# Optimization experiments

Hardware: AMD Instinct MI355X
Metric: run time of the kernel (lower is better)

The kernel has to match this reference:

```python
import jax, jax.numpy as jnp
import numpy as np

EPS = 1e-5  # torch nn.LayerNorm default


def layer_norm(x, g, b):
    mu = jnp.mean(x, axis=-1, keepdims=True)
    var = jnp.mean(jnp.square(x - mu), axis=-1, keepdims=True)
    return (x - mu) * jax.lax.rsqrt(var + EPS) * g + b


def run_dir(g_ih_seq, w_hh, g_hh, b_hh, g_ho, b_ho, reverse):
    """Run one LayerNormLSTMCell direction over precomputed LN(x @ W_ih^T).
    g_ih_seq: [S, B, 4H]. Returns final hidden [B, H]."""
    S, B, G = g_ih_seq.shape
    H = G // 4

    def step(carry, gih_t):
        h, c = carry
        gates = gih_t + layer_norm(h @ w_hh.T, g_hh, b_hh)  # [B, 4H]
        i, f, o = jnp.split(jax.nn.sigmoid(gates[:, : 3 * H]), 3, axis=1)
        g = jnp.tanh(gates[:, 3 * H :])
        c = f * c + i * g
        h = o * jnp.tanh(layer_norm(c, g_ho, b_ho))
        return (h, c), None

    z = jnp.zeros((B, H), g_ih_seq.dtype)
    (hT, _), _ = jax.lax.scan(step, (z, z), g_ih_seq, reverse=reverse)
    return hT


def lnlstm(x, w_ih0, w_hh0, ln_ih0_g, ln_ih0_b, ln_hh0_g, ln_hh0_b, ln_ho0_g,
           ln_ho0_b, w_ih1, w_hh1, ln_ih1_g, ln_ih1_b, ln_hh1_g, ln_hh1_b,
           ln_ho1_g, ln_ho1_b):
    # x: [B, S, E] -> permute(1,0,2)
    x_seq = jnp.transpose(x, (1, 0, 2))  # [S, B, E]
    S, B, _ = x_seq.shape

    # ---- layer 0 (time-varying input) ----
    g0f = layer_norm(jnp.einsum('sbe,ge->sbg', x_seq, w_ih0[0]), ln_ih0_g[0], ln_ih0_b[0])
    hf = run_dir(g0f, w_hh0[0], ln_hh0_g[0], ln_hh0_b[0], ln_ho0_g[0], ln_ho0_b[0], False)
    g0b = layer_norm(jnp.einsum('sbe,ge->sbg', x_seq, w_ih0[1]), ln_ih0_g[1], ln_ih0_b[1])
    hb = run_dir(g0b, w_hh0[1], ln_hh0_g[1], ln_hh0_b[1], ln_ho0_g[1], ln_ho0_b[1], True)

    # Due to the `[[None]*N]*seq_len` aliasing bug in the original torch code,
    # the next layer's input is the SAME vector at every timestep:
    xc = jnp.concatenate([hf, hb], axis=1)  # [B, 2H]

    # ---- layer 1 (constant input; LN(x@W_ih^T) computed once, broadcast over time) ----
    g1f = layer_norm(xc @ w_ih1[0].T, ln_ih1_g[0], ln_ih1_b[0])
    hf1 = run_dir(jnp.broadcast_to(g1f, (S,) + g1f.shape), w_hh1[0],
                  ln_hh1_g[0], ln_hh1_b[0], ln_ho1_g[0], ln_ho1_b[0], False)
    g1b = layer_norm(xc @ w_ih1[1].T, ln_ih1_g[1], ln_ih1_b[1])
    hb1 = run_dir(jnp.broadcast_to(g1b, (S,) + g1b.shape), w_hh1[1],
                  ln_hh1_g[1], ln_hh1_b[1], ln_ho1_g[1], ln_ho1_b[1], True)

    # y = max over time of identical vectors == the vector itself
    return jnp.concatenate([hf1, hb1], axis=1)  # [B, 2H]


def setup_inputs() -> dict:
    key = jax.random.key(0)
    ks = jax.random.split(key, 20)
    B, S, E, H = 64, 48, 512, 512
    f = jnp.float32
    n = jax.random.normal
    u = jax.random.uniform
    return {
        'x': n(ks[0], (B, S, E), f),
        'text_length': jax.random.randint(ks[1], (B,), 1, S),
        'w_ih0': n(ks[2], (2, 4 * H, E), f) * 0.05,
        'w_hh0': n(ks[3], (2, 4 * H, H), f) * 0.05,
        'ln_ih0_g': u(ks[4], (2, 4 * H), f, 0.5, 1.5),
        'ln_ih0_b': n(ks[5], (2, 4 * H), f) * 0.02,
        'ln_hh0_g': u(ks[6], (2, 4 * H), f, 0.5, 1.5),
        'ln_hh0_b': n(ks[7], (2, 4 * H), f) * 0.02,
        'ln_ho0_g': u(ks[8], (2, H), f, 0.5, 1.5),
        'ln_ho0_b': n(ks[9], (2, H), f) * 0.02,
        'w_ih1': n(ks[10], (2, 4 * H, 2 * H), f) * 0.05,
        'w_hh1': n(ks[11], (2, 4 * H, H), f) * 0.05,
        'ln_ih1_g': u(ks[12], (2, 4 * H), f, 0.5, 1.5),
        'ln_ih1_b': n(ks[13], (2, 4 * H), f) * 0.02,
        'ln_hh1_g': u(ks[14], (2, 4 * H), f, 0.5, 1.5),
        'ln_hh1_b': n(ks[15], (2, 4 * H), f) * 0.02,
        'ln_ho1_g': u(ks[16], (2, H), f, 0.5, 1.5),
        'ln_ho1_b': n(ks[17], (2, H), f) * 0.02,
    }


def reference(x, text_length, w_ih0, w_hh0, ln_ih0_g, ln_ih0_b, ln_hh0_g,
              ln_hh0_b, ln_ho0_g, ln_ho0_b, w_ih1, w_hh1, ln_ih1_g, ln_ih1_b,
              ln_hh1_g, ln_hh1_b, ln_ho1_g, ln_ho1_b):
    # text_length is accepted but unused by the original forward
    return lnlstm(x, w_ih0, w_hh0, ln_ih0_g, ln_ih0_b, ln_hh0_g, ln_hh0_b,
                  ln_ho0_g, ln_ho0_b, w_ih1, w_hh1, ln_ih1_g, ln_ih1_b,
                  ln_hh1_g, ln_hh1_b, ln_ho1_g, ln_ho1_b)
```

## Files before the change

kernel.cpp:

```cpp
#include <hip/hip_runtime.h>
#include <math.h>

#define HH 512
#define BB 64
#define SS 48
#define EE 512
#define G4 2048
#define EPSF 1e-5f
#define AGENT __HIP_MEMORY_SCOPE_AGENT
typedef unsigned long long ull;

__device__ __forceinline__ float aload(const float* p) {
  return __hip_atomic_load(p, __ATOMIC_RELAXED, AGENT);
}
__device__ __forceinline__ void astore(float* p, float v) {
  __hip_atomic_store(p, v, __ATOMIC_RELAXED, AGENT);
}
__device__ __forceinline__ float2 aloadf2(const float2* p) {
  ull u = __hip_atomic_load((const ull*)p, __ATOMIC_RELAXED, AGENT);
  union { ull u; float2 f; } x; x.u = u; return x.f;
}
__device__ __forceinline__ void astoref2(float2* p, float2 v) {
  union { ull u; float2 f; } x; x.f = v;
  __hip_atomic_store((ull*)p, x.u, __ATOMIC_RELAXED, AGENT);
}

__device__ __forceinline__ float fsig(float x) {
  x = fminf(fmaxf(x, -30.f), 30.f);
  return 1.f / (1.f + __expf(-x));
}
__device__ __forceinline__ float ftanh(float x) {
  float e = __expf(fminf(fmaxf(2.f*x, -60.f), 60.f));
  return (e - 1.f) / (e + 1.f);
}

__device__ __forceinline__ void wdetect(const int* f, int target) {
  int spins = 0;
  for (;;) {
    int v = __hip_atomic_load(f + (threadIdx.x & 31)*32, __ATOMIC_RELAXED, AGENT);
    #pragma unroll
    for (int off = 16; off > 0; off >>= 1) v = min(v, __shfl_xor(v, off, 32));
    if (v >= target) break;
    __builtin_amdgcn_s_sleep(1);
    if (++spins > (1 << 22)) break;
  }
}

__device__ __forceinline__ void gsync(int* c, int target) {
  __builtin_amdgcn_s_waitcnt(0);
  __syncthreads();
  if (threadIdx.x == 0) {
    __hip_atomic_fetch_add(c, 1, __ATOMIC_RELEASE, AGENT);
    int spins = 0;
    while (__hip_atomic_load(c, __ATOMIC_RELAXED, AGENT) < target) {
      __builtin_amdgcn_s_sleep(2);
      if (++spins > (1 << 21)) break;
    }
    (void)__hip_atomic_load(c, __ATOMIC_ACQUIRE, AGENT);
  }
  __syncthreads();
}

__global__ __launch_bounds__(256)
void gemm_ih0(const float* __restrict__ x, const float* __restrict__ w_ih0,
              float* __restrict__ G0) {
  __shared__ float As[16][65];
  __shared__ float Bs[16][65];
  const int m0 = blockIdx.y * 64;
  const int d  = m0 / (BB * SS);
  const float* Wm = w_ih0 + (size_t)d * G4 * EE;
  const int bn = blockIdx.x * 64;
  const int tid = threadIdx.x;
  const int lrow = tid >> 2;
  const int lkk  = (tid & 3) << 2;
  const int tx = tid & 15;
  const int ty = tid >> 4;
  int m  = m0 + lrow;
  int r  = m - d * (BB * SS);
  int b  = r / SS;
  int tl = r - b * SS;
  int s  = d ? (SS - 1 - tl) : tl;
  const float* arow = x + ((size_t)b * SS + s) * EE;

  float acc[4][4] = {};
  for (int k0 = 0; k0 < EE; k0 += 16) {
    float4 av = *(const float4*)(arow + k0 + lkk);
    float4 bv = *(const float4*)(Wm + (size_t)(bn + lrow) * EE + k0 + lkk);
    As[lkk+0][lrow] = av.x; As[lkk+1][lrow] = av.y; As[lkk+2][lrow] = av.z; As[lkk+3][lrow] = av.w;
    Bs[lkk+0][lrow] = bv.x; Bs[lkk+1][lrow] = bv.y; Bs[lkk+2][lrow] = bv.z; Bs[lkk+3][lrow] = bv.w;
    __syncthreads();
    #pragma unroll
    for (int k = 0; k < 16; ++k) {
      float a[4], bbv[4];
      #pragma unroll
      for (int i = 0; i < 4; ++i) a[i] = As[k][ty*4+i];
      #pragma unroll
      for (int j = 0; j < 4; ++j) bbv[j] = Bs[k][tx*4+j];
      #pragma unroll
      for (int i = 0; i < 4; ++i)
        #pragma unroll
        for (int j = 0; j < 4; ++j) acc[i][j] += a[i]*bbv[j];
    }
    __syncthreads();
  }
  for (int i = 0; i < 4; ++i)
    for (int j = 0; j < 4; ++j)
      G0[(size_t)(m0 + ty*4 + i) * G4 + bn + tx*4 + j] = acc[i][j];
}

__global__ __launch_bounds__(256)
void ln_rows(float* __restrict__ X, const float* __restrict__ gamma,
             const float* __restrict__ beta, int rows_per_d) {
  __shared__ float red[8];
  const int row = blockIdx.x;
  const int d = row / rows_per_d;
  float* xr = X + (size_t)row * G4;
  const float* gg = gamma + (size_t)d * G4;
  const float* bb = beta  + (size_t)d * G4;
  float s = 0.f, q = 0.f;
  float v[8];
  #pragma unroll
  for (int it = 0; it < 8; ++it) {
    float xv = xr[threadIdx.x + it*256];
    v[it] = xv; s += xv; q += xv*xv;
  }
  #pragma unroll
  for (int off = 32; off > 0; off >>= 1) { s += __shfl_down(s, off); q += __shfl_down(q, off); }
  int lane = threadIdx.x & 63, wid = threadIdx.x >> 6;
  if (lane == 0) { red[wid] = s; red[4+wid] = q; }
  __syncthreads();
  float ts = red[0]+red[1]+red[2]+red[3];
  float tq = red[4]+red[5]+red[6]+red[7];
  float mu = ts * (1.f/G4);
  float rstd = rsqrtf(tq*(1.f/G4) - mu*mu + EPSF);
  #pragma unroll
  for (int it = 0; it < 8; ++it) {
    int jc = threadIdx.x + it*256;
    xr[jc] = (v[it]-mu)*rstd*gg[jc] + bb[jc];
  }
}

__global__ __launch_bounds__(1024, 4)
void persist8(const float* __restrict__ whh, const float* __restrict__ Gbuf,
              long g_row_stride, long g_t_stride,
              const float* __restrict__ lnhg, const float* __restrict__ lnhb,
              const float* __restrict__ lnog, const float* __restrict__ lnob,
              float2* cobuf, float2* Rpart, float2* Cpart,
              int* flagsA, int* flagsB,
              float* fout, int nsteps,
              int mode1, const float* __restrict__ w_ih1,
              const float* __restrict__ xcb, float* g1pre,
              const float* __restrict__ ln_g1, const float* __restrict__ ln_b1,
              int* cnt_pre) {
  __shared__ float hlds[16][1024];
  __shared__ float part[16][8][64];
  __shared__ float redR[16][64];
  __shared__ float sred[32];

  const int bb = blockIdx.x;
  const int tid = threadIdx.x;
  const int l = tid & 63;

  if (mode1) {
    const int dp = bb & 1, nbp = bb >> 1;
    const int pb = tid >> 4, ns = tid & 15;
    const int col = nbp*16 + ns;
    const float* xrow = xcb + (size_t)pb * 1024;
    const float* wv_ = w_ih1 + ((size_t)dp*G4 + col) * 1024;
    float a = 0.f;
    for (int k = 0; k < 1024; k += 4) {
      float4 xv = *(const float4*)(xrow + k);
      float4 wv4 = *(const float4*)(wv_ + k);
      a += xv.x*wv4.x + xv.y*wv4.y + xv.z*wv4.z + xv.w*wv4.w;
    }
    astore(g1pre + ((size_t)dp*BB + pb) * G4 + col, a);
    gsync(cnt_pre + 0, 256);
    if (bb < 128) {
      const int ld = bb >> 6;
      float* xr = g1pre + (size_t)bb * G4;
      const float* gg = ln_g1 + (size_t)ld * G4;
      const float* be = ln_b1 + (size_t)ld * G4;
      float v0 = aload(xr + tid), v1 = aload(xr + tid + 1024);
      float s = v0 + v1, q = v0*v0 + v1*v1;
      #pragma unroll
      for (int off = 32; off > 0; off >>= 1) { s += __shfl_down(s, off); q += __shfl_down(q, off); }
      const int wv2 = tid >> 6;
      if (l == 0) { sred[wv2] = s; sred[16+wv2] = q; }
      __syncthreads();
      float ts = 0.f, tq = 0.f;
      #pragma unroll
      for (int i = 0; i < 16; ++i) { ts += sred[i]; tq += sred[16+i]; }
      float mu = ts * (1.f/G4);
      float rstd = rsqrtf(tq*(1.f/G4) - mu*mu + EPSF);
      astore(xr + tid,        (v0-mu)*rstd*gg[tid]      + be[tid]);
      astore(xr + tid + 1024, (v1-mu)*rstd*gg[tid+1024] + be[tid+1024]);
    }
    gsync(cnt_pre + 16, 256);
  }

  const int g  = bb & 7;
  const int d  = g >> 2;
  const int bq = g & 3;
  const int jb = bb >> 3;
  const int rowbase = d*BB + bq*16;
  const int ke = tid >> 6;
  const int ncol = jb*16 + ((l>>4) << 9) + (l & 15);
  int* fA = flagsA + g*1024;
  int* fB = flagsB + g*1024;

  float wreg[32];
  {
    const float* wp = whh + ((size_t)d*G4 + ncol)*HH + (size_t)ke*32;
    #pragma unroll
    for (int i = 0; i < 32; ++i) wreg[i] = wp[i];
  }

  const int bl = tid >> 4, jl = tid & 15;
  const int rowc = rowbase + bl;
  const int jc = jb*16 + jl;
  const int scol = tid & 511, srh = tid >> 9;
  const float ogv = lnog[(size_t)d*HH + scol];
  const float obv = lnob[(size_t)d*HH + scol];
  const int row16 = tid >> 5, j32 = tid & 31;
  const int inv_g = (g_t_stride == 0);
  const int strow = rowbase + ((l >> 3) << 1) + srh;
  const int stslot = (l & 7) * 4;

  float hg0=0,hg1=0,hg2=0,hg3=0, hb0=0,hb1=0,hb2=0,hb3=0;
  float cg0=0,cg1=0,cg2=0,cg3=0;
  if (tid < 256) {
    const float* lnhg_d = lnhg + (size_t)d*G4;
    const float* lnhb_d = lnhb + (size_t)d*G4;
    hg0 = lnhg_d[jc];        hb0 = lnhb_d[jc];
    hg1 = lnhg_d[HH+jc];     hb1 = lnhb_d[HH+jc];
    hg2 = lnhg_d[2*HH+jc];   hb2 = lnhb_d[2*HH+jc];
    hg3 = lnhg_d[3*HH+jc];   hb3 = lnhb_d[3*HH+jc];
    if (inv_g) {
      const float* gr = Gbuf + (size_t)rowc * g_row_stride;
      cg0 = gr[jc]; cg1 = gr[HH+jc]; cg2 = gr[2*HH+jc]; cg3 = gr[3*HH+jc];
    }
  }
  float creg = 0.f;

  for (int t = 0; t < nsteps; ++t) {
    wdetect(fB, t);
    {
      float2 co[8];
      #pragma unroll
      for (int i = 0; i < 8; ++i)
        co[i] = aloadf2(cobuf + (size_t)(rowbase + i*2 + srh)*512 + scol);
      float s = 0.f, q = 0.f;
      #pragma unroll
      for (int m = 0; m < 4; ++m) {
        float2 p = aloadf2(Cpart + (size_t)strow*32 + stslot + m);
        s += p.x; q += p.y;
      }
      #pragma unroll
      for (int off = 4; off > 0; off >>= 1) { s += __shfl_xor(s, off, 8); q += __shfl_xor(q, off, 8); }
      #pragma unroll
      for (int i = 0; i < 8; ++i) {
        float si = __shfl(s, i*8, 64);
        float qi = __shfl(q, i*8, 64);
        float mu = si * (1.f/HH);
        float rs = rsqrtf(qi*(1.f/HH) - mu*mu + EPSF);
        hlds[i*2 + srh][scol] = co[i].y * ftanh((co[i].x - mu)*rs*ogv + obv);
      }
    }
    __syncthreads();

    #pragma unroll
    for (int half = 0; half < 2; ++half) {
      #pragma unroll
      for (int b = 0; b < 8; ++b) {
        const float* hp = &hlds[half*8 + b][ke*32];
        float acc = 0.f;
        #pragma unroll
        for (int i4 = 0; i4 < 8; ++i4) {
          float4 h4 = *(const float4*)(hp + 4*i4);
          acc += h4.x*wreg[4*i4+0] + h4.y*wreg[4*i4+1]
               + h4.z*wreg[4*i4+2] + h4.w*wreg[4*i4+3];
        }
        part[ke][b][l] = acc;
      }
      __syncthreads();
      if (tid < 512) {
        int b = tid >> 6, n2 = tid & 63;
        float r = 0.f;
        #pragma unroll
        for (int k16 = 0; k16 < 16; ++k16) r += part[k16][b][n2];
        redR[half*8 + b][n2] = r;
      }
      __syncthreads();
    }
    if (tid < 512) {
      float v1 = redR[row16][j32], v2 = redR[row16][j32+32];
      float s = v1 + v2, q = v1*v1 + v2*v2;
      #pragma unroll
      for (int off = 16; off > 0; off >>= 1) { s += __shfl_down(s, off, 32); q += __shfl_down(q, off, 32); }
      if (j32 == 0)
        astoref2(Rpart + (size_t)(rowbase+row16)*32 + jb, make_float2(s, q));
    }
    float pg0 = cg0, pg1 = cg1, pg2 = cg2, pg3 = cg3;
    if (tid < 256 && !inv_g) {
      const float* gr = Gbuf + (size_t)rowc * g_row_stride + (size_t)t * g_t_stride;
      pg0 = gr[jc]; pg1 = gr[HH+jc]; pg2 = gr[2*HH+jc]; pg3 = gr[3*HH+jc];
    }
    __syncthreads();
    if (tid == 0) __hip_atomic_store(fA + jb*32, t + 1, __ATOMIC_RELAXED, AGENT);

    if (tid < 256) {
      wdetect(fA, t + 1);
      float2 pa = aloadf2(Rpart + (size_t)rowc*32 + jl);
      float2 pb = aloadf2(Rpart + (size_t)rowc*32 + jl + 16);
      float s2 = pa.x + pb.x, q2 = pa.y + pb.y;
      #pragma unroll
      for (int off = 8; off > 0; off >>= 1) { s2 += __shfl_xor(s2, off, 16); q2 += __shfl_xor(q2, off, 16); }
      float mu = s2 * (1.f/G4);
      float rstd = rsqrtf(q2*(1.f/G4) - mu*mu + EPSF);
      float gi = pg0 + (redR[bl][jl]    - mu)*rstd*hg0 + hb0;
      float gf = pg1 + (redR[bl][16+jl] - mu)*rstd*hg1 + hb1;
      float go = pg2 + (redR[bl][32+jl] - mu)*rstd*hg2 + hb2;
      float gt = pg3 + (redR[bl][48+jl] - mu)*rstd*hg3 + hb3;
      float iv = fsig(gi), fv = fsig(gf), ov = fsig(go), gv = ftanh(gt);
      creg = fv*creg + iv*gv;
      float cs = creg, cq = creg*creg;
      #pragma unroll
      for (int off = 8; off > 0; off >>= 1) { cs += __shfl_xor(cs, off, 16); cq += __shfl_xor(cq, off, 16); }
      if (jl == 0)
        astoref2(Cpart + (size_t)rowc*32 + jb, make_float2(cs, cq));
      astoref2(cobuf + (size_t)rowc*512 + jc, make_float2(creg, ov));
    }
    __syncthreads();
    if (tid == 0) __hip_atomic_store(fB + jb*32, t + 1, __ATOMIC_RELAXED, AGENT);
  }

  if (jb == 0) {
    wdetect(fB, nsteps);
    float2 co[8];
    #pragma unroll
    for (int i = 0; i < 8; ++i)
      co[i] = aloadf2(cobuf + (size_t)(rowbase + i*2 + srh)*512 + scol);
    float s = 0.f, q = 0.f;
    #pragma unroll
    for (int m = 0; m < 4; ++m) {
      float2 p = aloadf2(Cpart + (size_t)strow*32 + stslot + m);
      s += p.x; q += p.y;
    }
    #pragma unroll
    for (int off = 4; off > 0; off >>= 1) { s += __shfl_xor(s, off, 8); q += __shfl_xor(q, off, 8); }
    #pragma unroll
    for (int i = 0; i < 8; ++i) {
      float si = __shfl(s, i*8, 64);
      float qi = __shfl(q, i*8, 64);
      float mu = si * (1.f/HH);
      float rs = rsqrtf(qi*(1.f/HH) - mu*mu + EPSF);
      int row = i*2 + srh;
      float h = co[i].y * ftanh((co[i].x - mu)*rs*ogv + obv);
      fout[(size_t)(bq*16 + row) * 1024 + (size_t)d*512 + scol] = h;
    }
  }
}

extern "C" void kernel_launch(void* const* d_in, const int* in_sizes, int n_in,
                              void* d_out, int out_size, void* d_ws, size_t ws_size,
                              hipStream_t stream) {
  const float* x        = (const float*)d_in[0];
  const float* w_ih0    = (const float*)d_in[2];
  const float* w_hh0    = (const float*)d_in[3];
  const float* ln_ih0_g = (const float*)d_in[4];
  const float* ln_ih0_b = (const float*)d_in[5];
  const float* ln_hh0_g = (const float*)d_in[6];
  const float* ln_hh0_b = (const float*)d_in[7];
  const float* ln_ho0_g = (const float*)d_in[8];
  const float* ln_ho0_b = (const float*)d_in[9];
  const float* w_ih1    = (const float*)d_in[10];
  const float* w_hh1    = (const float*)d_in[11];
  const float* ln_ih1_g = (const float*)d_in[12];
  const float* ln_ih1_b = (const float*)d_in[13];
  const float* ln_hh1_g = (const float*)d_in[14];
  const float* ln_hh1_b = (const float*)d_in[15];
  const float* ln_ho1_g = (const float*)d_in[16];
  const float* ln_ho1_b = (const float*)d_in[17];
  float* out = (float*)d_out;

  float*  G0    = (float*)d_ws;
  float*  g1pre = G0 + (size_t)2*BB*SS*G4;
  float*  xcb   = g1pre + (size_t)2*BB*G4;
  float2* Rpart = (float2*)(xcb + (size_t)BB*1024);
  float2* Cpart = Rpart + (size_t)128*32;
  float2* cobuf = Cpart + (size_t)128*32;
  int*    ints  = (int*)(cobuf + (size_t)128*512);
  int*    fA0     = ints;
  int*    fB0     = ints + 8192;
  int*    fA1     = ints + 16384;
  int*    fB1     = ints + 24576;
  int*    cnt_pre = ints + 32768;

  hipMemsetAsync(Cpart, 0, ((size_t)128*32 + (size_t)128*512)*sizeof(float2)
                           + 32832*sizeof(int), stream);

  hipLaunchKernelGGL(gemm_ih0, dim3(G4/64, (2*BB*SS)/64), dim3(256), 0, stream,
      x, w_ih0, G0);
  hipLaunchKernelGGL(ln_rows, dim3(2*BB*SS), dim3(256), 0, stream,
      G0, ln_ih0_g, ln_ih0_b, BB*SS);

  hipLaunchKernelGGL(persist8, dim3(256), dim3(1024), 0, stream,
      w_hh0, G0, (long)SS*G4, (long)G4,
      ln_hh0_g, ln_hh0_b, ln_ho0_g, ln_ho0_b,
      cobuf, Rpart, Cpart, fA0, fB0, xcb, SS,
      0, (const float*)nullptr, (const float*)nullptr, (float*)nullptr,
      (const float*)nullptr, (const float*)nullptr, (int*)nullptr);

  hipMemsetAsync(Cpart, 0, ((size_t)128*32 + (size_t)128*512)*sizeof(float2), stream);

  hipLaunchKernelGGL(persist8, dim3(256), dim3(1024), 0, stream,
      w_hh1, g1pre, (long)G4, 0L,
      ln_hh1_g, ln_hh1_b, ln_ho1_g, ln_ho1_b,
      cobuf, Rpart, Cpart, fA1, fB1, out, SS,
      1, w_ih1, xcb, g1pre, ln_ih1_g, ln_ih1_b, cnt_pre);
}
```

Measured before the change: 1.896 ms.

## Split each block's work across both directions to overlap phase-A barrier latency

Each persistent block now handles 8 batch rows from each of the two LSTM directions instead of 16 rows from one direction. It keeps both directions' recurrent weight slices in registers. Each step runs the forward-direction matvec and publishes its partial stats with flag fA0, then does the backward-direction matvec while that flag propagates, so the grid-wide wait is hidden behind useful work. The cost is twice the weight registers per thread (risking spills or lower occupancy at 1024 threads), more __syncthreads per step, and a larger flag layout.

```diff
diff --git a/kernel.cpp b/kernel.cpp
--- a/kernel.cpp
+++ b/kernel.cpp
@@ -141,20 +141,21 @@
 }
 
 __global__ __launch_bounds__(1024, 4)
-void persist8(const float* __restrict__ whh, const float* __restrict__ Gbuf,
+void persist9(const float* __restrict__ whh, const float* __restrict__ Gbuf,
               long g_row_stride, long g_t_stride,
               const float* __restrict__ lnhg, const float* __restrict__ lnhb,
               const float* __restrict__ lnog, const float* __restrict__ lnob,
               float2* cobuf, float2* Rpart, float2* Cpart,
-              int* flagsA, int* flagsB,
-              float* fout, int nsteps,
+              int* flags, float* fout, int nsteps,
               int mode1, const float* __restrict__ w_ih1,
               const float* __restrict__ xcb, float* g1pre,
               const float* __restrict__ ln_g1, const float* __restrict__ ln_b1,
               int* cnt_pre) {
-  __shared__ float hlds[16][1024];
+  __shared__ float hlds0[8][1024];
+  __shared__ float hlds1[8][1024];
   __shared__ float part[16][8][64];
-  __shared__ float redR[16][64];
+  __shared__ float redR0[8][64];
+  __shared__ float redR1[8][64];
   __shared__ float sred[32];
 
   const int bb = blockIdx.x;
@@ -199,45 +200,48 @@
   }
 
   const int g  = bb & 7;
-  const int d  = g >> 2;
-  const int bq = g & 3;
   const int jb = bb >> 3;
-  const int rowbase = d*BB + bq*16;
+  const int brow0 = g*8;
+  const int brow1 = 64 + g*8;
   const int ke = tid >> 6;
   const int ncol = jb*16 + ((l>>4) << 9) + (l & 15);
-  int* fA = flagsA + g*1024;
-  int* fB = flagsB + g*1024;
-
-  float wreg[32];
+  int* fA0 = flags + g*3072;
+  int* fA1 = fA0 + 1024;
+  int* fB  = fA0 + 2048;
+
+  float wreg0[32], wreg1[32];
   {
-    const float* wp = whh + ((size_t)d*G4 + ncol)*HH + (size_t)ke*32;
-    #pragma unroll
-    for (int i = 0; i < 32; ++i) wreg[i] = wp[i];
-  }
-
-  const int bl = tid >> 4, jl = tid & 15;
-  const int rowc = rowbase + bl;
-  const int jc = jb*16 + jl;
+    const float* wp0 = whh + (size_t)ncol*HH + (size_t)ke*32;
+    const float* wp1 = whh + (size_t)(G4 + ncol)*HH + (size_t)ke*32;
+    #pragma unroll
+    for (int i = 0; i < 32; ++i) { wreg0[i] = wp0[i]; wreg1[i] = wp1[i]; }
+  }
+
   const int scol = tid & 511, srh = tid >> 9;
-  const float ogv = lnog[(size_t)d*HH + scol];
-  const float obv = lnob[(size_t)d*HH + scol];
-  const int row16 = tid >> 5, j32 = tid & 31;
+  const float ogv0 = lnog[scol],      obv0 = lnob[scol];
+  const float ogv1 = lnog[HH + scol], obv1 = lnob[HH + scol];
+  const int strow = l >> 3;
+  const int stslot = (l & 7) * 4;
   const int inv_g = (g_t_stride == 0);
-  const int strow = rowbase + ((l >> 3) << 1) + srh;
-  const int stslot = (l & 7) * 4;
-
+
+  int urowc = 0, ujc = 0, ubl = 0, ujl = 0;
   float hg0=0,hg1=0,hg2=0,hg3=0, hb0=0,hb1=0,hb2=0,hb3=0;
   float cg0=0,cg1=0,cg2=0,cg3=0;
   if (tid < 256) {
-    const float* lnhg_d = lnhg + (size_t)d*G4;
-    const float* lnhb_d = lnhb + (size_t)d*G4;
-    hg0 = lnhg_d[jc];        hb0 = lnhb_d[jc];
-    hg1 = lnhg_d[HH+jc];     hb1 = lnhb_d[HH+jc];
-    hg2 = lnhg_d[2*HH+jc];   hb2 = lnhb_d[2*HH+jc];
-    hg3 = lnhg_d[3*HH+jc];   hb3 = lnhb_d[3*HH+jc];
+    const int ud = tid >> 7;
+    const int u = tid & 127;
+    ubl = u >> 4; ujl = u & 15;
+    urowc = ud*64 + g*8 + ubl;
+    ujc = jb*16 + ujl;
+    const float* hgp = lnhg + (size_t)ud*G4;
+    const float* hbp = lnhb + (size_t)ud*G4;
+    hg0 = hgp[ujc];        hb0 = hbp[ujc];
+    hg1 = hgp[HH+ujc];     hb1 = hbp[HH+ujc];
+    hg2 = hgp[2*HH+ujc];   hb2 = hbp[2*HH+ujc];
+    hg3 = hgp[3*HH+ujc];   hb3 = hbp[3*HH+ujc];
     if (inv_g) {
-      const float* gr = Gbuf + (size_t)rowc * g_row_stride;
-      cg0 = gr[jc]; cg1 = gr[HH+jc]; cg2 = gr[2*HH+jc]; cg3 = gr[3*HH+jc];
+      const float* gr = Gbuf + (size_t)urowc * g_row_stride;
+      cg0 = gr[ujc]; cg1 = gr[HH+ujc]; cg2 = gr[2*HH+ujc]; cg3 = gr[3*HH+ujc];
     }
   }
   float creg = 0.f;
@@ -245,90 +249,142 @@
   for (int t = 0; t < nsteps; ++t) {
     wdetect(fB, t);
     {
-      float2 co[8];
-      #pragma unroll
-      for (int i = 0; i < 8; ++i)
-        co[i] = aloadf2(cobuf + (size_t)(rowbase + i*2 + srh)*512 + scol);
-      float s = 0.f, q = 0.f;
+      float2 co[4]; float s = 0.f, q = 0.f;
+      #pragma unroll
+      for (int i = 0; i < 4; ++i)
+        co[i] = aloadf2(cobuf + (size_t)(brow0 + i*2 + srh)*512 + scol);
       #pragma unroll
       for (int m = 0; m < 4; ++m) {
-        float2 p = aloadf2(Cpart + (size_t)strow*32 + stslot + m);
+        float2 p = aloadf2(Cpart + (size_t)(brow0 + strow)*32 + stslot + m);
         s += p.x; q += p.y;
       }
       #pragma unroll
       for (int off = 4; off > 0; off >>= 1) { s += __shfl_xor(s, off, 8); q += __shfl_xor(q, off, 8); }
       #pragma unroll
-      for (int i = 0; i < 8; ++i) {
-        float si = __shfl(s, i*8, 64);
-        float qi = __shfl(q, i*8, 64);
+      for (int i = 0; i < 4; ++i) {
+        int r = i*2 + srh;
+        float si = __shfl(s, r*8, 64), qi = __shfl(q, r*8, 64);
         float mu = si * (1.f/HH);
         float rs = rsqrtf(qi*(1.f/HH) - mu*mu + EPSF);
-        hlds[i*2 + srh][scol] = co[i].y * ftanh((co[i].x - mu)*rs*ogv + obv);
-      }
-    }
-    __syncthreads();
-
-    #pragma unroll
-    for (int half = 0; half < 2; ++half) {
-      #pragma unroll
-      for (int b = 0; b < 8; ++b) {
-        const float* hp = &hlds[half*8 + b][ke*32];
-        float acc = 0.f;
-        #pragma unroll
-        for (int i4 = 0; i4 < 8; ++i4) {
-          float4 h4 = *(const float4*)(hp + 4*i4);
-          acc += h4.x*wreg[4*i4+0] + h4.y*wreg[4*i4+1]
-               + h4.z*wreg[4*i4+2] + h4.w*wreg[4*i4+3];
-        }
-        part[ke][b][l] = acc;
-      }
-      __syncthreads();
-      if (tid < 512) {
-        int b = tid >> 6, n2 = tid & 63;
-        float r = 0.f;
-        #pragma unroll
-        for (int k16 = 0; k16 < 16; ++k16) r += part[k16][b][n2];
-        redR[half*8 + b][n2] = r;
-      }
-      __syncthreads();
-    }
+        hlds0[r][scol] = co[i].y * ftanh((co[i].x - mu)*rs*ogv0 + obv0);
+      }
+    }
+    __syncthreads();
+    #pragma unroll
+    for (int b = 0; b < 8; ++b) {
+      const float* hp = &hlds0[b][ke*32];
+      float acc = 0.f;
+      #pragma unroll
+      for (int i4 = 0; i4 < 8; ++i4) {
+        float4 h4 = *(const float4*)(hp + 4*i4);
+        acc += h4.x*wreg0[4*i4+0] + h4.y*wreg0[4*i4+1]
+             + h4.z*wreg0[4*i4+2] + h4.w*wreg0[4*i4+3];
+      }
+      part[ke][b][l] = acc;
+    }
+    __syncthreads();
     if (tid < 512) {
-      float v1 = redR[row16][j32], v2 = redR[row16][j32+32];
+      int b = tid >> 6, n2 = tid & 63;
+      float r = 0.f;
+      #pragma unroll
+      for (int k16 = 0; k16 < 16; ++k16) r += part[k16][b][n2];
+      redR0[b][n2] = r;
+    }
+    __syncthreads();
+    if (tid < 256) {
+      int row8 = tid >> 5, j32 = tid & 31;
+      float v1 = redR0[row8][j32], v2 = redR0[row8][j32+32];
       float s = v1 + v2, q = v1*v1 + v2*v2;
       #pragma unroll
       for (int off = 16; off > 0; off >>= 1) { s += __shfl_down(s, off, 32); q += __shfl_down(q, off, 32); }
       if (j32 == 0)
-        astoref2(Rpart + (size_t)(rowbase+row16)*32 + jb, make_float2(s, q));
+        astoref2(Rpart + (size_t)(brow0 + row8)*32 + jb, make_float2(s, q));
     }
     float pg0 = cg0, pg1 = cg1, pg2 = cg2, pg3 = cg3;
     if (tid < 256 && !inv_g) {
-      const float* gr = Gbuf + (size_t)rowc * g_row_stride + (size_t)t * g_t_stride;
-      pg0 = gr[jc]; pg1 = gr[HH+jc]; pg2 = gr[2*HH+jc]; pg3 = gr[3*HH+jc];
-    }
-    __syncthreads();
-    if (tid == 0) __hip_atomic_store(fA + jb*32, t + 1, __ATOMIC_RELAXED, AGENT);
-
+      const float* gr = Gbuf + (size_t)urowc * g_row_stride + (size_t)t * g_t_stride;
+      pg0 = gr[ujc]; pg1 = gr[HH+ujc]; pg2 = gr[2*HH+ujc]; pg3 = gr[3*HH+ujc];
+    }
+    __syncthreads();
+    if (tid == 0) __hip_atomic_store(fA0 + jb*32, t + 1, __ATOMIC_RELAXED, AGENT);
+
+    {
+      float2 co[4]; float s = 0.f, q = 0.f;
+      #pragma unroll
+      for (int i = 0; i < 4; ++i)
+        co[i] = aloadf2(cobuf + (size_t)(brow1 + i*2 + srh)*512 + scol);
+      #pragma unroll
+      for (int m = 0; m < 4; ++m) {
+        float2 p = aloadf2(Cpart + (size_t)(brow1 + strow)*32 + stslot + m);
+        s += p.x; q += p.y;
+      }
+      #pragma unroll
+      for (int off = 4; off > 0; off >>= 1) { s += __shfl_xor(s, off, 8); q += __shfl_xor(q, off, 8); }
+      #pragma unroll
+      for (int i = 0; i < 4; ++i) {
+        int r = i*2 + srh;
+        float si = __shfl(s, r*8, 64), qi = __shfl(q, r*8, 64);
+        float mu = si * (1.f/HH);
+        float rs = rsqrtf(qi*(1.f/HH) - mu*mu + EPSF);
+        hlds1[r][scol] = co[i].y * ftanh((co[i].x - mu)*rs*ogv1 + obv1);
+      }
+    }
+    __syncthreads();
+    #pragma unroll
+    for (int b = 0; b < 8; ++b) {
+      const float* hp = &hlds1[b][ke*32];
+      float acc = 0.f;
+      #pragma unroll
+      for (int i4 = 0; i4 < 8; ++i4) {
+        float4 h4 = *(const float4*)(hp + 4*i4);
+        acc += h4.x*wreg1[4*i4+0] + h4.y*wreg1[4*i4+1]
+             + h4.z*wreg1[4*i4+2] + h4.w*wreg1[4*i4+3];
+      }
+      part[ke][b][l] = acc;
+    }
+    __syncthreads();
+    if (tid < 512) {
+      int b = tid >> 6, n2 = tid & 63;
+      float r = 0.f;
+      #pragma unroll
+      for (int k16 = 0; k16 < 16; ++k16) r += part[k16][b][n2];
+      redR1[b][n2] = r;
+    }
+    __syncthreads();
     if (tid < 256) {
-      wdetect(fA, t + 1);
-      float2 pa = aloadf2(Rpart + (size_t)rowc*32 + jl);
-      float2 pb = aloadf2(Rpart + (size_t)rowc*32 + jl + 16);
-      float s2 = pa.x + pb.x, q2 = pa.y + pb.y;
+      int row8 = tid >> 5, j32 = tid & 31;
+      float v1 = redR1[row8][j32], v2 = redR1[row8][j32+32];
+      float s = v1 + v2, q = v1*v1 + v2*v2;
+      #pragma unroll
+      for (int off = 16; off > 0; off >>= 1) { s += __shfl_down(s, off, 32); q += __shfl_down(q, off, 32); }
+      if (j32 == 0)
+        astoref2(Rpart + (size_t)(brow1 + row8)*32 + jb, make_float2(s, q));
+    }
+    __syncthreads();
+    if (tid == 0) __hip_atomic_store(fA1 + jb*32, t + 1, __ATOMIC_RELAXED, AGENT);
+
+    if (tid < 256) {
+      const float (*redR)[64] = (tid < 128) ? redR0 : redR1;
+      wdetect((tid < 128) ? fA0 : fA1, t + 1);
+      float2 pa = aloadf2(Rpart + (size_t)urowc*32 + ujl);
+      float2 pb2 = aloadf2(Rpart + (size_t)urowc*32 + ujl + 16);
+      float s2 = pa.x + pb2.x, q2 = pa.y + pb2.y;
       #pragma unroll
       for (int off = 8; off > 0; off >>= 1) { s2 += __shfl_xor(s2, off, 16); q2 += __shfl_xor(q2, off, 16); }
       float mu = s2 * (1.f/G4);
       float rstd = rsqrtf(q2*(1.f/G4) - mu*mu + EPSF);
-      float gi = pg0 + (redR[bl][jl]    - mu)*rstd*hg0 + hb0;
-      float gf = pg1 + (redR[bl][16+jl] - mu)*rstd*hg1 + hb1;
-      float go = pg2 + (redR[bl][32+jl] - mu)*rstd*hg2 + hb2;
-      float gt = pg3 + (redR[bl][48+jl] - mu)*rstd*hg3 + hb3;
+      float gi = pg0 + (redR[ubl][ujl]    - mu)*rstd*hg0 + hb0;
+      float gf = pg1 + (redR[ubl][16+ujl] - mu)*rstd*hg1 + hb1;
+      float go = pg2 + (redR[ubl][32+ujl] - mu)*rstd*hg2 + hb2;
+      float gt = pg3 + (redR[ubl][48+ujl] - mu)*rstd*hg3 + hb3;
       float iv = fsig(gi), fv = fsig(gf), ov = fsig(go), gv = ftanh(gt);
       creg = fv*creg + iv*gv;
       float cs = creg, cq = creg*creg;
       #pragma unroll
       for (int off = 8; off > 0; off >>= 1) { cs += __shfl_xor(cs, off, 16); cq += __shfl_xor(cq, off, 16); }
-      if (jl == 0)
-        astoref2(Cpart + (size_t)rowc*32 + jb, make_float2(cs, cq));
-      astoref2(cobuf + (size_t)rowc*512 + jc, make_float2(creg, ov));
+      if (ujl == 0)
+        astoref2(Cpart + (size_t)urowc*32 + jb, make_float2(cs, cq));
+      astoref2(cobuf + (size_t)urowc*512 + ujc, make_float2(creg, ov));
     }
     __syncthreads();
     if (tid == 0) __hip_atomic_store(fB + jb*32, t + 1, __ATOMIC_RELAXED, AGENT);
@@ -336,27 +392,31 @@
 
   if (jb == 0) {
     wdetect(fB, nsteps);
-    float2 co[8];
-    #pragma unroll
-    for (int i = 0; i < 8; ++i)
-      co[i] = aloadf2(cobuf + (size_t)(rowbase + i*2 + srh)*512 + scol);
-    float s = 0.f, q = 0.f;
-    #pragma unroll
-    for (int m = 0; m < 4; ++m) {
-      float2 p = aloadf2(Cpart + (size_t)strow*32 + stslot + m);
-      s += p.x; q += p.y;
-    }
-    #pragma unroll
-    for (int off = 4; off > 0; off >>= 1) { s += __shfl_xor(s, off, 8); q += __shfl_xor(q, off, 8); }
-    #pragma unroll
-    for (int i = 0; i < 8; ++i) {
-      float si = __shfl(s, i*8, 64);
-      float qi = __shfl(q, i*8, 64);
-      float mu = si * (1.f/HH);
-      float rs = rsqrtf(qi*(1.f/HH) - mu*mu + EPSF);
-      int row = i*2 + srh;
-      float h = co[i].y * ftanh((co[i].x - mu)*rs*ogv + obv);
-      fout[(size_t)(bq*16 + row) * 1024 + (size_t)d*512 + scol] = h;
+    #pragma unroll
+    for (int dd = 0; dd < 2; ++dd) {
+      const int base = dd*64 + g*8;
+      const float og = dd ? ogv1 : ogv0;
+      const float ob = dd ? obv1 : obv0;
+      float2 co[4]; float s = 0.f, q = 0.f;
+      #pragma unroll
+      for (int i = 0; i < 4; ++i)
+        co[i] = aloadf2(cobuf + (size_t)(base + i*2 + srh)*512 + scol);
+      #pragma unroll
+      for (int m = 0; m < 4; ++m) {
+        float2 p = aloadf2(Cpart + (size_t)(base + strow)*32 + stslot + m);
+        s += p.x; q += p.y;
+      }
+      #pragma unroll
+      for (int off = 4; off > 0; off >>= 1) { s += __shfl_xor(s, off, 8); q += __shfl_xor(q, off, 8); }
+      #pragma unroll
+      for (int i = 0; i < 4; ++i) {
+        int r = i*2 + srh;
+        float si = __shfl(s, r*8, 64), qi = __shfl(q, r*8, 64);
+        float mu = si * (1.f/HH);
+        float rs = rsqrtf(qi*(1.f/HH) - mu*mu + EPSF);
+        float h = co[i].y * ftanh((co[i].x - mu)*rs*og + ob);
+        fout[(size_t)(g*8 + r)*1024 + (size_t)dd*512 + scol] = h;
+      }
     }
   }
 }
@@ -390,32 +450,30 @@
   float2* Cpart = Rpart + (size_t)128*32;
   float2* cobuf = Cpart + (size_t)128*32;
   int*    ints  = (int*)(cobuf + (size_t)128*512);
-  int*    fA0     = ints;
-  int*    fB0     = ints + 8192;
-  int*    fA1     = ints + 16384;
-  int*    fB1     = ints + 24576;
-  int*    cnt_pre = ints + 32768;
+  int*    flagsL0 = ints;
+  int*    flagsL1 = ints + 24576;
+  int*    cnt_pre = ints + 49152;
 
   hipMemsetAsync(Cpart, 0, ((size_t)128*32 + (size_t)128*512)*sizeof(float2)
-                           + 32832*sizeof(int), stream);
+                           + (49152 + 64)*sizeof(int), stream);
 
   hipLaunchKernelGGL(gemm_ih0, dim3(G4/64, (2*BB*SS)/64), dim3(256), 0, stream,
       x, w_ih0, G0);
   hipLaunchKernelGGL(ln_rows, dim3(2*BB*SS), dim3(256), 0, stream,
       G0, ln_ih0_g, ln_ih0_b, BB*SS);
 
-  hipLaunchKernelGGL(persist8, dim3(256), dim3(1024), 0, stream,
+  hipLaunchKernelGGL(persist9, dim3(256), dim3(1024), 0, stream,
       w_hh0, G0, (long)SS*G4, (long)G4,
       ln_hh0_g, ln_hh0_b, ln_ho0_g, ln_ho0_b,
-      cobuf, Rpart, Cpart, fA0, fB0, xcb, SS,
+      cobuf, Rpart, Cpart, flagsL0, xcb, SS,
       0, (const float*)nullptr, (const float*)nullptr, (float*)nullptr,
       (const float*)nullptr, (const float*)nullptr, (int*)nullptr);
 
   hipMemsetAsync(Cpart, 0, ((size_t)128*32 + (size_t)128*512)*sizeof(float2), stream);
 
-  hipLaunchKernelGGL(persist8, dim3(256), dim3(1024), 0, stream,
+  hipLaunchKernelGGL(persist9, dim3(256), dim3(1024), 0, stream,
       w_hh1, g1pre, (long)G4, 0L,
       ln_hh1_g, ln_hh1_b, ln_ho1_g, ln_ho1_b,
-      cobuf, Rpart, Cpart, fA1, fB1, out, SS,
+      cobuf, Rpart, Cpart, flagsL1, out, SS,
       1, w_ih1, xcb, g1pre, ln_ih1_g, ln_ih1_b, cnt_pre);
 }
```

New measurement: 2.714 ms. 1.43x slower.
